# Kernel tuning notes

Measured on AMD Instinct MI355X. Metric: run time of the kernel, lower is better.

The kernel has to match this reference:

```python
import jax, jax.numpy as jnp
import numpy as np

VOCAB_SIZE = 4096
D_EMBED = 256
BETA = 0.25  # unused: module returns raw commit_loss; beta applied by caller


def setup_inputs() -> dict:
    key = jax.random.key(0)
    k_h, k_e = jax.random.split(key)
    h = jax.random.normal(k_h, (16, D_EMBED, 32, 32), dtype=jnp.float32)
    embedding = jax.random.normal(k_e, (VOCAB_SIZE, D_EMBED), dtype=jnp.float32)
    return {"h": h, "embedding": embedding}


def reference(h, embedding):
    B, C, H, W = h.shape
    h = h.astype(jnp.float32)
    # (B, C, H, W) -> (N, C) with N = B*H*W
    h_flat = jnp.transpose(h, (0, 2, 3, 1)).reshape(-1, C)
    dist = (
        jnp.sum(h_flat * h_flat, axis=1, keepdims=True)
        + jnp.sum(embedding * embedding, axis=1)
        - 2.0 * jnp.einsum("nc,vc->nv", h_flat, embedding)
    )
    indices_flat = jnp.argmin(dist, axis=1)
    indices = indices_flat.reshape(B, H, W)
    # gather codebook vectors and restore (B, C, H, W)
    z_q = jnp.transpose(embedding[indices_flat].reshape(B, H, W, C), (0, 3, 1, 2))
    commit_loss = jnp.mean((h - jax.lax.stop_gradient(z_q)) ** 2)
    # straight-through estimator
    z_q_st = h + jax.lax.stop_gradient(z_q - h)
    return z_q_st, indices, commit_loss
```

## Files before the change

### kernel.cpp

```cpp
#include <hip/hip_runtime.h>

#define D 256
#define VOCAB 4096
#define NTOT 16384
#define N_OUT0 4194304

typedef _Float16 half8 __attribute__((ext_vector_type(8)));
typedef float f32x4 __attribute__((ext_vector_type(4)));
typedef unsigned long long u64;

__device__ __forceinline__ void gld16(const void* g, void* l) {
    __builtin_amdgcn_global_load_lds(
        (const __attribute__((address_space(1))) void*)g,
        (__attribute__((address_space(3))) void*)l, 16, 0, 0);
}

__device__ __forceinline__ u64 pack_key(float d, int v) {
    unsigned u = __float_as_uint(d);
    u ^= ((unsigned)((int)u >> 31)) | 0x80000000u;
    return ((u64)u << 32) | (unsigned)v;
}

__device__ __forceinline__ float unpack_dist(u64 k) {
    unsigned u = (unsigned)(k >> 32);
    u = (u & 0x80000000u) ? (u ^ 0x80000000u) : ~u;
    return __uint_as_float(u);
}

__global__ __launch_bounds__(256) void k_pack(const float* __restrict__ h,
                                              const float* __restrict__ emb,
                                              _Float16* __restrict__ Apk,
                                              _Float16* __restrict__ Bpk,
                                              float* __restrict__ hsqp,
                                              float* __restrict__ ht,
                                              float* __restrict__ esq,
                                              float* __restrict__ e2maxp,
                                              float* __restrict__ out2) {
    __shared__ float S[8192];
    const int tid = threadIdx.x;
    const int bid = blockIdx.x;
    if (bid < 512) {
        const int bm = bid >> 3, w = bid & 7;
        const int b = bm >> 2, p0 = (bm & 3) * 256;
        const float* src = h + ((size_t)b << 18) + p0;
#pragma unroll 4
        for (int cl = 0; cl < 32; ++cl)
            S[cl * 256 + tid] = src[(size_t)(w * 32 + cl) << 10 | (unsigned)tid];
        __syncthreads();
        float sq = 0.0f;
#pragma unroll
        for (int cl = 0; cl < 32; ++cl) {
            float t = S[cl * 256 + tid];
            sq = fmaf(t, t, sq);
        }
        hsqp[(size_t)(bm * 8 + w) * 256 + tid] = sq;
        float* htr = ht + ((size_t)(bm * 256 + tid)) * D + w * 32;
#pragma unroll
        for (int c4 = 0; c4 < 8; ++c4) {
            float4 t;
            t.x = S[(c4 * 4 + 0) * 256 + tid];
            t.y = S[(c4 * 4 + 1) * 256 + tid];
            t.z = S[(c4 * 4 + 2) * 256 + tid];
            t.w = S[(c4 * 4 + 3) * 256 + tid];
            *(float4*)(htr + c4 * 4) = t;
        }
        _Float16* dstT = Apk + (size_t)bm * 65536 + (size_t)w * 8192;
#pragma unroll
        for (int i = 0; i < 4; ++i) {
            alignas(16) _Float16 hi[8];
#pragma unroll
            for (int j = 0; j < 8; ++j) hi[j] = (_Float16)S[(i * 8 + j) * 256 + tid];
            *(half8*)(dstT + i * 2048 + tid * 8) = *(half8*)hi;
        }
    } else if (bid < 768) {
        const int bid2 = bid - 512;
        const int bn = bid2 >> 3, w = bid2 & 7;
        const int v0 = bn * 128;
#pragma unroll 4
        for (int i = 0; i < 16; ++i) {
            int flat = i * 256 + tid;
            int r = flat >> 5, cl = flat & 31;
            S[cl * 129 + r] = emb[(size_t)(v0 + r) * D + w * 32 + cl];
        }
        __syncthreads();
        _Float16* dstT = Bpk + (size_t)bn * 32768 + (size_t)w * 4096;
#pragma unroll
        for (int i = 0; i < 2; ++i) {
            int s = i * 256 + tid;
            int q = s >> 7, r = s & 127;
            alignas(16) _Float16 hi[8];
#pragma unroll
            for (int j = 0; j < 8; ++j) hi[j] = (_Float16)S[(q * 8 + j) * 129 + r];
            *(half8*)(dstT + q * 1024 + r * 8) = *(half8*)hi;
        }
    } else {
        __shared__ float sm[4];
        const int pid = bid - 768;
        const int lane = tid & 63, wv = tid >> 6;
        const int v0 = pid * 64;
        float lmax = 0.0f;
#pragma unroll 4
        for (int i = 0; i < 16; ++i) {
            int v = v0 + i * 4 + wv;
            float4 e = *(const float4*)(emb + (size_t)v * D + lane * 4);
            float s = e.x * e.x + e.y * e.y + e.z * e.z + e.w * e.w;
#pragma unroll
            for (int m = 32; m >= 1; m >>= 1) s += __shfl_xor(s, m, 64);
            if (lane == 0) esq[v] = s;
            lmax = fmaxf(lmax, s);
        }
        if (lane == 0) sm[wv] = lmax;
        __syncthreads();
        if (tid == 0) {
            e2maxp[pid] = fmaxf(fmaxf(sm[0], sm[1]), fmaxf(sm[2], sm[3]));
            if (pid == 0) out2[0] = 0.0f;
        }
    }
}


#define STAGE(W, BUF) do { \
    _Pragma("unroll") \
    for (int s_ = 0; s_ < 2; ++s_) { \
        int f_ = s_ * 256 + tid; \
        gld16(AgH + (W) * 8192 + (f_ >> 7) * 2048 + (f_ & 127) * 8, \
              As + (BUF) * 4096 + f_ * 8); \
    } \
    _Pragma("unroll") \
    for (int s_ = 0; s_ < 2; ++s_) { \
        int f_ = s_ * 256 + tid; \
        gld16(Bg + (W) * 4096 + f_ * 8, Bs + (BUF) * 4096 + f_ * 8); \
    } } while (0)

#define PHASE_END(N) do { \
    __builtin_amdgcn_sched_barrier(0); \
    asm volatile("s_waitcnt vmcnt(" #N ")" ::: "memory"); \
    __builtin_amdgcn_s_barrier(); } while (0)

#define WINDOW(BUF, DOSTAGE, SW, SBUF) do { \
    const _Float16* aB = As + (BUF) * 4096 + quad * 1024 + (wm * 64 + j16) * 8; \
    const _Float16* bB = Bs + (BUF) * 4096 + quad * 1024 + (wn * 64 + j16) * 8; \
    if (DOSTAGE) STAGE(SW, SBUF); \
    half8 af[4], bf[4]; \
    _Pragma("unroll") \
    for (int mt_ = 0; mt_ < 4; ++mt_) af[mt_] = *(const half8*)(aB + mt_ * 128); \
    _Pragma("unroll") \
    for (int nt_ = 0; nt_ < 4; ++nt_) bf[nt_] = *(const half8*)(bB + nt_ * 128); \
    __builtin_amdgcn_s_setprio(1); \
    _Pragma("unroll") \
    for (int mt_ = 0; mt_ < 4; ++mt_) { \
      _Pragma("unroll") \
      for (int nt_ = 0; nt_ < 4; ++nt_) \
        acc[mt_][nt_] = __builtin_amdgcn_mfma_f32_16x16x32_f16(af[mt_], bf[nt_], acc[mt_][nt_], 0, 0, 0); \
    } \
    __builtin_amdgcn_s_setprio(0); \
  } while (0)

__global__ __launch_bounds__(256, 3) void k_gemm(const _Float16* __restrict__ Apk,
                                                 const _Float16* __restrict__ Bpk,
                                                 const float* __restrict__ esq,
                                                 u64* __restrict__ keys2) {
    __shared__ alignas(16) char smem[49152];
    _Float16* As = (_Float16*)smem;
    _Float16* Bs = (_Float16*)(smem + 24576);

    const int tid = threadIdx.x;
    const int bid = blockIdx.x;
    const int swz = (bid & 7) * 512 + (bid >> 3);
    const int bm = swz >> 5, bn = swz & 31;
    const int m0 = bm * 128, n0 = bn * 128;

    const _Float16* AgH = Apk + (size_t)(bm >> 1) * 65536 + (size_t)(bm & 1) * 1024;
    const _Float16* Bg = Bpk + (size_t)bn * 32768;

    STAGE(0, 0);
    STAGE(1, 1);

    const int wv = tid >> 6, l = tid & 63;
    const int wm = wv & 1, wn = wv >> 1;
    const int quad = l >> 4, j16 = l & 15;

    f32x4 acc[4][4];
#pragma unroll
    for (int i = 0; i < 4; ++i)
#pragma unroll
        for (int j = 0; j < 4; ++j) acc[i][j] = (f32x4)0.0f;

    asm volatile("s_waitcnt vmcnt(4)" ::: "memory");
    __builtin_amdgcn_s_barrier();

    WINDOW(0, 1, 2, 2); PHASE_END(4);
    WINDOW(1, 1, 3, 0); PHASE_END(4);
    WINDOW(2, 1, 4, 1); PHASE_END(4);
    WINDOW(0, 1, 5, 2); PHASE_END(4);
    WINDOW(1, 1, 6, 0); PHASE_END(4);
    WINDOW(2, 1, 7, 1); PHASE_END(4);
    WINDOW(0, 0, 0, 0); PHASE_END(0);
    WINDOW(1, 0, 0, 0);
    __syncthreads();

    u64* t2 = (u64*)smem;
    float es[4];
    int vidx[4];
#pragma unroll
    for (int nt = 0; nt < 4; ++nt) {
        vidx[nt] = n0 + wn * 64 + nt * 16 + j16;
        es[nt] = esq[vidx[nt]];
    }

    u64 M1 = ~0ULL, M2 = ~0ULL;
#pragma unroll
    for (int pass = 0; pass < 2; ++pass) {
        if (wn == pass) {
#pragma unroll
            for (int mt = 0; mt < 4; ++mt) {
#pragma unroll
                for (int r = 0; r < 4; ++r) {
                    float d1 = __builtin_inff(), d2 = __builtin_inff();
                    int i1 = 0, i2 = 0;
#pragma unroll
                    for (int nt = 0; nt < 4; ++nt) {
                        float dv = es[nt] - 2.0f * acc[mt][nt][r];
                        bool c1 = dv < d1;
                        bool c2 = dv < d2;
                        d2 = c1 ? d1 : (c2 ? dv : d2);
                        i2 = c1 ? i1 : (c2 ? vidx[nt] : i2);
                        d1 = c1 ? dv : d1;
                        i1 = c1 ? vidx[nt] : i1;
                    }
                    int row = wm * 64 + mt * 16 + quad * 4 + r;
                    u64* p = t2 + ((size_t)(row * 16 + (j16 ^ (row & 7))) * 2);
                    p[0] = pack_key(d1, i1);
                    p[1] = pack_key(d2, i2);
                }
            }
        }
        __syncthreads();
        if (tid < 128) {
            const int row = tid;
#pragma unroll
            for (int j = 0; j < 16; ++j) {
                const u64* p = t2 + ((size_t)(row * 16 + (j ^ (row & 7))) * 2);
                u64 a1 = p[0], a2 = p[1];
                u64 x = M1 > a1 ? M1 : a1;
                M1 = M1 < a1 ? M1 : a1;
                u64 y = M2 < a2 ? M2 : a2;
                M2 = x < y ? x : y;
            }
        }
        __syncthreads();
    }
    if (tid < 128) {
        keys2[(size_t)(m0 + tid) * 64 + bn * 2 + 0] = M1;
        keys2[(size_t)(m0 + tid) * 64 + bn * 2 + 1] = M2;
    }
}

__device__ __forceinline__ u64 exact_key_ht(const float* __restrict__ ht,
                                            const float* __restrict__ emb,
                                            const float* __restrict__ esq,
                                            int rg, int v, int lane) {
    const float4 h4 = *(const float4*)(ht + (size_t)rg * D + lane * 4);
    const float4 e4 = *(const float4*)(emb + (size_t)v * D + lane * 4);
    float p = h4.x * e4.x;
    p = fmaf(h4.y, e4.y, p);
    p = fmaf(h4.z, e4.z, p);
    p = fmaf(h4.w, e4.w, p);
#pragma unroll
    for (int m = 32; m >= 1; m >>= 1) p += __shfl_xor(p, m, 64);
    return pack_key(esq[v] - 2.0f * p, v);
}

__global__ __launch_bounds__(256) void k_refine(const float* __restrict__ ht,
                                                const float* __restrict__ emb,
                                                const float* __restrict__ esq,
                                                const float* __restrict__ hsqp,
                                                const float* __restrict__ e2maxp,
                                                const u64* __restrict__ keys2,
                                                float* __restrict__ out1) {
    __shared__ float sE2;
    const int tid = threadIdx.x;
    const int lane = tid & 63;
    const int w = tid >> 6;
    const int n0 = blockIdx.x * 32;

    if (tid < 64) {
        float m = e2maxp[tid];
#pragma unroll
        for (int s = 32; s >= 1; s >>= 1) m = fmaxf(m, __shfl_xor(m, s, 64));
        if (tid == 0) sE2 = m;
    }
    __syncthreads();
    const float e2m = sE2;

    int rg = n0 + w * 8;
    u64 key = keys2[(size_t)rg * 64 + lane];
#pragma unroll 1
    for (int rr = 0; rr < 8; ++rr, ++rg) {
        u64 keyn = 0;
        if (rr < 7) keyn = keys2[(size_t)(rg + 1) * 64 + lane];
        u64 gm = key;
#pragma unroll
        for (int m = 32; m >= 1; m >>= 1) {
            u64 o = __shfl_xor(gm, m, 64);
            gm = o < gm ? o : gm;
        }
        float hq = 0.0f;
#pragma unroll
        for (int k = 0; k < 8; ++k) hq += hsqp[(size_t)(rg >> 8) * 2048 + k * 256 + (rg & 255)];
        const float thr = unpack_dist(gm) + 4.0e-3f * sqrtf(hq * e2m) + 1e-2f;
        u64 cmask = __ballot(unpack_dist(key) <= thr);
        u64 bestk;
        if (__popcll(cmask) == 1) {
            bestk = gm;
        } else {
            bestk = ~0ULL;
            u64 rescan = 0;
            u64 cm = cmask;
            while (cm) {
                int L = __ffsll((long long)cm) - 1;
                cm &= cm - 1;
                if (L & 1) {
                    rescan |= 1ull << (L >> 1);
                } else {
                    u64 kL = __shfl(key, L, 64);
                    u64 ek = exact_key_ht(ht, emb, esq, rg, (int)(kL & 0xFFFFFFFFu), lane);
                    bestk = ek < bestk ? ek : bestk;
                }
            }
            while (rescan) {
                int bnr = __ffsll((long long)rescan) - 1;
                rescan &= rescan - 1;
                const float* htr = ht + (size_t)rg * D;
                u64 k0 = ~0ULL, k1 = ~0ULL;
#pragma unroll
                for (int c = 0; c < 2; ++c) {
                    int v = bnr * 128 + c * 64 + lane;
                    float p = 0.0f;
#pragma unroll 8
                    for (int d = 0; d < D; d += 4) {
                        float4 hh = *(const float4*)(htr + d);
                        float4 ee = *(const float4*)(emb + (size_t)v * D + d);
                        p = fmaf(hh.x, ee.x, p);
                        p = fmaf(hh.y, ee.y, p);
                        p = fmaf(hh.z, ee.z, p);
                        p = fmaf(hh.w, ee.w, p);
                    }
                    u64 kc = pack_key(esq[v] - 2.0f * p, v);
                    if (c == 0) k0 = kc; else k1 = kc;
                }
                u64 m1 = k0 < k1 ? k0 : k1, m2 = k0 < k1 ? k1 : k0;
#pragma unroll
                for (int m = 32; m >= 1; m >>= 1) {
                    u64 o1 = __shfl_xor(m1, m, 64), o2 = __shfl_xor(m2, m, 64);
                    u64 hi = m1 > o1 ? m1 : o1;
                    m1 = m1 < o1 ? m1 : o1;
                    u64 lo2 = m2 < o2 ? m2 : o2;
                    m2 = hi < lo2 ? hi : lo2;
                }
                u64 e1 = exact_key_ht(ht, emb, esq, rg, (int)(m1 & 0xFFFFFFFFu), lane);
                u64 e2 = exact_key_ht(ht, emb, esq, rg, (int)(m2 & 0xFFFFFFFFu), lane);
                bestk = e1 < bestk ? e1 : bestk;
                bestk = e2 < bestk ? e2 : bestk;
            }
        }
        if (lane == 0) out1[rg] = (float)(int)(bestk & 0xFFFFFFFFu);
        key = keyn;
    }
}

__global__ __launch_bounds__(256) void k_out(const float* __restrict__ h,
                                             const float* __restrict__ emb,
                                             const float* __restrict__ out1,
                                             float* __restrict__ out0,
                                             float* __restrict__ out2) {
    __shared__ float zq[32][260];
    __shared__ float wred[4];
    const int tid = threadIdx.x;
    const int lane = tid & 63;
    const int w = tid >> 6;
    const int n0 = blockIdx.x * 32;
    const int b = n0 >> 10;
    const int p0 = n0 & 1023;
#pragma unroll
    for (int rr = 0; rr < 8; ++rr) {
        int r = w * 8 + rr;
        unsigned idx = (unsigned)(int)out1[n0 + r];
        float4 e4 = *(const float4*)(emb + (size_t)idx * D + lane * 4);
        *(float4*)&zq[r][lane * 4] = e4;
    }
    __syncthreads();
    float lsum = 0.0f;
    const size_t base = ((size_t)b * D) << 10;
#pragma unroll 4
    for (int it = 0; it < 32; ++it) {
        int c = it * 8 + (tid >> 5);
        int pp = tid & 31;
        float z = zq[pp][c];
        size_t g = base + ((size_t)c << 10) + p0 + pp;
        float hv = h[g];
        out0[g] = hv + (z - hv);
        float d = hv - z;
        lsum = fmaf(d, d, lsum);
    }
#pragma unroll
    for (int m = 32; m >= 1; m >>= 1) lsum += __shfl_xor(lsum, m, 64);
    if (lane == 0) wred[w] = lsum;
    __syncthreads();
    if (tid == 0)
        atomicAdd(out2, (wred[0] + wred[1] + wred[2] + wred[3]) * (1.0f / (float)N_OUT0));
}

extern "C" void kernel_launch(void* const* d_in, const int* in_sizes, int n_in,
                              void* d_out, int out_size, void* d_ws, size_t ws_size,
                              hipStream_t stream) {
    const float* h = (const float*)d_in[0];
    const float* emb = (const float*)d_in[1];
    float* out0 = (float*)d_out;
    float* out1 = out0 + N_OUT0;
    float* out2 = out1 + NTOT;

    char* wsb = (char*)d_ws;
    _Float16* Apk = (_Float16*)wsb;
    _Float16* Bpk = (_Float16*)(wsb + 8388608);
    float* esq = (float*)(wsb + 10485760);
    float* hsqp = (float*)(wsb + 10502144);
    float* e2maxp = (float*)(wsb + 11026432);
    u64* keys2 = (u64*)(wsb + 11028480);

    hipLaunchKernelGGL(k_pack, dim3(832), dim3(256), 0, stream, h, emb, Apk, Bpk, hsqp, out0, esq, e2maxp, out2);
    hipLaunchKernelGGL(k_gemm, dim3(4096), dim3(256), 0, stream, Apk, Bpk, esq, keys2);
    hipLaunchKernelGGL(k_refine, dim3(NTOT / 32), dim3(256), 0, stream, out0, emb, esq, hsqp, e2maxp, keys2, out1);
    hipLaunchKernelGGL(k_out, dim3(NTOT / 32), dim3(256), 0, stream, h, emb, out1, out0, out2);
}
```

Measured before the change: 190.0 us.

## Load GEMM operands directly from global into registers, dropping LDS staging

Replaces the LDS triple-buffered global_load_lds pipeline in the distance GEMM with direct per-lane global loads of MFMA fragments, double-buffered in registers. Shared memory is cut to the key table used by the argmin epilogue, and the per-window barriers are removed. The aim is lower synchronization overhead and higher occupancy. The cost is that tiles shared across waves are now fetched redundantly from global/L2 with no LDS reuse, and register pressure rises from the prefetch buffers.

```diff
diff --git a/kernel.cpp b/kernel.cpp
--- a/kernel.cpp
+++ b/kernel.cpp
@@ -8,12 +8,6 @@
 typedef _Float16 half8 __attribute__((ext_vector_type(8)));
 typedef float f32x4 __attribute__((ext_vector_type(4)));
 typedef unsigned long long u64;
-
-__device__ __forceinline__ void gld16(const void* g, void* l) {
-    __builtin_amdgcn_global_load_lds(
-        (const __attribute__((address_space(1))) void*)g,
-        (__attribute__((address_space(3))) void*)l, 16, 0, 0);
-}
 
 __device__ __forceinline__ u64 pack_key(float d, int v) {
     unsigned u = __float_as_uint(d);
@@ -118,51 +112,11 @@
     }
 }
 
-
-#define STAGE(W, BUF) do { \
-    _Pragma("unroll") \
-    for (int s_ = 0; s_ < 2; ++s_) { \
-        int f_ = s_ * 256 + tid; \
-        gld16(AgH + (W) * 8192 + (f_ >> 7) * 2048 + (f_ & 127) * 8, \
-              As + (BUF) * 4096 + f_ * 8); \
-    } \
-    _Pragma("unroll") \
-    for (int s_ = 0; s_ < 2; ++s_) { \
-        int f_ = s_ * 256 + tid; \
-        gld16(Bg + (W) * 4096 + f_ * 8, Bs + (BUF) * 4096 + f_ * 8); \
-    } } while (0)
-
-#define PHASE_END(N) do { \
-    __builtin_amdgcn_sched_barrier(0); \
-    asm volatile("s_waitcnt vmcnt(" #N ")" ::: "memory"); \
-    __builtin_amdgcn_s_barrier(); } while (0)
-
-#define WINDOW(BUF, DOSTAGE, SW, SBUF) do { \
-    const _Float16* aB = As + (BUF) * 4096 + quad * 1024 + (wm * 64 + j16) * 8; \
-    const _Float16* bB = Bs + (BUF) * 4096 + quad * 1024 + (wn * 64 + j16) * 8; \
-    if (DOSTAGE) STAGE(SW, SBUF); \
-    half8 af[4], bf[4]; \
-    _Pragma("unroll") \
-    for (int mt_ = 0; mt_ < 4; ++mt_) af[mt_] = *(const half8*)(aB + mt_ * 128); \
-    _Pragma("unroll") \
-    for (int nt_ = 0; nt_ < 4; ++nt_) bf[nt_] = *(const half8*)(bB + nt_ * 128); \
-    __builtin_amdgcn_s_setprio(1); \
-    _Pragma("unroll") \
-    for (int mt_ = 0; mt_ < 4; ++mt_) { \
-      _Pragma("unroll") \
-      for (int nt_ = 0; nt_ < 4; ++nt_) \
-        acc[mt_][nt_] = __builtin_amdgcn_mfma_f32_16x16x32_f16(af[mt_], bf[nt_], acc[mt_][nt_], 0, 0, 0); \
-    } \
-    __builtin_amdgcn_s_setprio(0); \
-  } while (0)
-
 __global__ __launch_bounds__(256, 3) void k_gemm(const _Float16* __restrict__ Apk,
                                                  const _Float16* __restrict__ Bpk,
                                                  const float* __restrict__ esq,
                                                  u64* __restrict__ keys2) {
-    __shared__ alignas(16) char smem[49152];
-    _Float16* As = (_Float16*)smem;
-    _Float16* Bs = (_Float16*)(smem + 24576);
+    __shared__ u64 t2[4096];
 
     const int tid = threadIdx.x;
     const int bid = blockIdx.x;
@@ -170,36 +124,50 @@
     const int bm = swz >> 5, bn = swz & 31;
     const int m0 = bm * 128, n0 = bn * 128;
 
-    const _Float16* AgH = Apk + (size_t)(bm >> 1) * 65536 + (size_t)(bm & 1) * 1024;
-    const _Float16* Bg = Bpk + (size_t)bn * 32768;
-
-    STAGE(0, 0);
-    STAGE(1, 1);
-
     const int wv = tid >> 6, l = tid & 63;
     const int wm = wv & 1, wn = wv >> 1;
     const int quad = l >> 4, j16 = l & 15;
 
+    const _Float16* aP = Apk + (size_t)(bm >> 1) * 65536 + (size_t)(bm & 1) * 1024
+                       + quad * 2048 + (wm * 64 + j16) * 8;
+    const _Float16* bP = Bpk + (size_t)bn * 32768
+                       + quad * 1024 + (wn * 64 + j16) * 8;
+
     f32x4 acc[4][4];
 #pragma unroll
     for (int i = 0; i < 4; ++i)
 #pragma unroll
         for (int j = 0; j < 4; ++j) acc[i][j] = (f32x4)0.0f;
 
-    asm volatile("s_waitcnt vmcnt(4)" ::: "memory");
-    __builtin_amdgcn_s_barrier();
-
-    WINDOW(0, 1, 2, 2); PHASE_END(4);
-    WINDOW(1, 1, 3, 0); PHASE_END(4);
-    WINDOW(2, 1, 4, 1); PHASE_END(4);
-    WINDOW(0, 1, 5, 2); PHASE_END(4);
-    WINDOW(1, 1, 6, 0); PHASE_END(4);
-    WINDOW(2, 1, 7, 1); PHASE_END(4);
-    WINDOW(0, 0, 0, 0); PHASE_END(0);
-    WINDOW(1, 0, 0, 0);
-    __syncthreads();
-
-    u64* t2 = (u64*)smem;
+    half8 af[4], bf[4], afn[4], bfn[4];
+#pragma unroll
+    for (int mt = 0; mt < 4; ++mt) af[mt] = *(const half8*)(aP + mt * 128);
+#pragma unroll
+    for (int nt = 0; nt < 4; ++nt) bf[nt] = *(const half8*)(bP + nt * 128);
+
+#pragma unroll
+    for (int w = 0; w < 8; ++w) {
+        if (w < 7) {
+#pragma unroll
+            for (int mt = 0; mt < 4; ++mt)
+                afn[mt] = *(const half8*)(aP + (w + 1) * 8192 + mt * 128);
+#pragma unroll
+            for (int nt = 0; nt < 4; ++nt)
+                bfn[nt] = *(const half8*)(bP + (w + 1) * 4096 + nt * 128);
+        }
+        __builtin_amdgcn_s_setprio(1);
+#pragma unroll
+        for (int mt = 0; mt < 4; ++mt)
+#pragma unroll
+            for (int nt = 0; nt < 4; ++nt)
+                acc[mt][nt] = __builtin_amdgcn_mfma_f32_16x16x32_f16(af[mt], bf[nt], acc[mt][nt], 0, 0, 0);
+        __builtin_amdgcn_s_setprio(0);
+#pragma unroll
+        for (int mt = 0; mt < 4; ++mt) af[mt] = afn[mt];
+#pragma unroll
+        for (int nt = 0; nt < 4; ++nt) bf[nt] = bfn[nt];
+    }
+
     float es[4];
     int vidx[4];
 #pragma unroll
```

New measurement: 181.3 us. 1.05x faster.
